# Kernel tuning notes

Hardware: AMD Instinct MI355X
Metric: run time of the kernel (lower is better)

## Reference

```python
import jax, jax.numpy as jnp
import numpy as np

N_NODES = 50000
N_EDGES = 800000
F_IN = 128
HID = 128
F_OUT = 2


def setup_inputs() -> dict:
    key = jax.random.key(0)
    ks = jax.random.split(key, 12)
    s = lambda d: 1.0 / np.sqrt(d)
    return {
        "x": jax.random.normal(ks[0], (N_NODES, F_IN), dtype=jnp.float32),
        "edge_index": jax.random.randint(ks[1], (2, N_EDGES), 0, N_NODES, dtype=jnp.int64),
        "W1_root": jax.random.normal(ks[2], (F_IN, HID), dtype=jnp.float32) * s(F_IN),
        "W1_nbr": jax.random.normal(ks[3], (F_IN, HID), dtype=jnp.float32) * s(F_IN),
        "b1": jnp.zeros((HID,), dtype=jnp.float32),
        "W2_root": jax.random.normal(ks[4], (HID, HID), dtype=jnp.float32) * s(HID),
        "W2_nbr": jax.random.normal(ks[5], (HID, HID), dtype=jnp.float32) * s(HID),
        "b2": jnp.zeros((HID,), dtype=jnp.float32),
        "Wa": jax.random.normal(ks[6], (HID, HID), dtype=jnp.float32) * s(HID),
        "a_src": jax.random.normal(ks[7], (HID,), dtype=jnp.float32) * s(HID),
        "a_dst": jax.random.normal(ks[8], (HID,), dtype=jnp.float32) * s(HID),
        "Wfc": jax.random.normal(ks[9], (HID, F_OUT), dtype=jnp.float32) * s(HID),
        "bfc": jnp.zeros((F_OUT,), dtype=jnp.float32),
    }


def reference(x, edge_index, W1_root, W1_nbr, b1, W2_root, W2_nbr, b2,
              Wa, a_src, a_dst, Wfc, bfc):
    src = edge_index[0]
    dst = edge_index[1]
    N = x.shape[0]

    def graph_conv(h, Wr, Wn, b):
        # sum-aggregate neighbor features, then two linear maps (PyG GraphConv)
        agg = jax.ops.segment_sum(h[src], dst, num_segments=N)  # [N, d]
        return h @ Wr + agg @ Wn + b

    h = jax.nn.relu(graph_conv(x, W1_root, W1_nbr, b1))
    h = jax.nn.relu(graph_conv(h, W2_root, W2_nbr, b2))

    # GAT-style attention: e_ij = LeakyReLU(a_src . Wh_j + a_dst . Wh_i)
    ht = h @ Wa                      # [N, HID]
    s_src = ht @ a_src               # [N]
    s_dst = ht @ a_dst               # [N]
    e = jax.nn.leaky_relu(s_src[src] + s_dst[dst], negative_slope=0.2)  # [E]

    # segment softmax over incoming edges of each destination node
    m = jax.ops.segment_max(e, dst, num_segments=N)          # [N]
    ee = jnp.exp(e - m[dst])                                  # [E]
    denom = jax.ops.segment_sum(ee, dst, num_segments=N)     # [N]
    alpha = ee / (denom[dst] + 1e-16)                         # [E]

    out = jax.ops.segment_sum(alpha[:, None] * ht[src], dst, num_segments=N)  # [N, HID]
    return out @ Wfc + bfc
```

## Files before the change

kernel.cpp:

```cpp
#include <hip/hip_runtime.h>
#include <cstddef>
#include <cstdint>


typedef __attribute__((ext_vector_type(8))) short short8;
typedef __attribute__((ext_vector_type(4))) float f32x4;

#define NBUK 128
#define BSH  9
#define CHUNK 1568

__device__ __forceinline__ ushort f2b(float f) {
  uint32_t u = __float_as_uint(f);
  u += 0x7fffu + ((u >> 16) & 1u);
  return (ushort)(u >> 16);
}
__device__ __forceinline__ float b2f(ushort h) {
  return __uint_as_float(((uint32_t)h) << 16);
}

__device__ __forceinline__ void gload_lds16(const void* g, void* l) {
  __builtin_amdgcn_global_load_lds(
      (const __attribute__((address_space(1))) void*)g,
      (__attribute__((address_space(3))) void*)l, 16, 0, 0);
}


__global__ __launch_bounds__(256) void split_kernel(
    const float* __restrict__ in, ushort* __restrict__ hi,
    ushort* __restrict__ lo, int n) {
  int i = (blockIdx.x * blockDim.x + threadIdx.x) * 8;
  if (i >= n) return;
  float4 v0 = *(const float4*)(in + i);
  float4 v1 = *(const float4*)(in + i + 4);
  float v[8] = {v0.x, v0.y, v0.z, v0.w, v1.x, v1.y, v1.z, v1.w};
  short8 h, l;
  #pragma unroll
  for (int b = 0; b < 8; ++b) {
    ushort hh = f2b(v[b]);
    h[b] = (short)hh;
    l[b] = (short)f2b(v[b] - b2f(hh));
  }
  *(short8*)(hi + i) = h;
  *(short8*)(lo + i) = l;
}


__global__ __launch_bounds__(256) void wsplit_kernel(
    const float* __restrict__ W0, const float* __restrict__ W1,
    const float* __restrict__ W2, const float* __restrict__ W3,
    const float* __restrict__ W4,
    ushort* __restrict__ WhT, ushort* __restrict__ WlT) {
  __shared__ float tile[128][128];
  int m = blockIdx.x;
  const float* W = (m == 0) ? W0 : (m == 1) ? W1 : (m == 2) ? W2 : (m == 3) ? W3 : W4;
  int t = threadIdx.x;
  #pragma unroll
  for (int i = 0; i < 64; ++i) {
    int idx = i * 256 + t;
    tile[idx >> 7][idx & 127] = W[idx];
  }
  __syncthreads();
  int j = t >> 1, k0 = (t & 1) * 64;
  size_t obase = (size_t)m * 16384 + (size_t)j * 128 + k0;
  #pragma unroll
  for (int c = 0; c < 8; ++c) {
    short8 h, l;
    #pragma unroll
    for (int b = 0; b < 8; ++b) {
      float v = tile[k0 + c * 8 + b][j];
      ushort hh = f2b(v);
      h[b] = (short)hh;
      l[b] = (short)f2b(v - b2f(hh));
    }
    *(short8*)(WhT + obase + c * 8) = h;
    *(short8*)(WlT + obase + c * 8) = l;
  }
}


__global__ __launch_bounds__(256) void bhist_kernel(
    const int* __restrict__ ei, int E, int* __restrict__ bcnt) {
  __shared__ int lh[NBUK];
  int t = threadIdx.x;
  if (t < NBUK) lh[t] = 0;
  __syncthreads();
  int base = blockIdx.x * CHUNK;
  int lim = base + CHUNK; if (lim > E) lim = E;
  for (int i = base + t; i < lim; i += 256) atomicAdd(&lh[ei[E + i] >> BSH], 1);
  __syncthreads();
  if (t < NBUK && lh[t]) atomicAdd(&bcnt[t], lh[t]);
}

__global__ __launch_bounds__(256) void bscan_kernel(
    const int* __restrict__ bcnt, int* __restrict__ bbase,
    int* __restrict__ gtail) {
  __shared__ int sA[NBUK], sB[NBUK];
  int t = threadIdx.x;
  if (t < NBUK) sA[t] = bcnt[t];
  __syncthreads();
  int *s = sA, *d = sB;
  for (int st = 1; st < NBUK; st <<= 1) {
    if (t < NBUK) d[t] = s[t] + ((t >= st) ? s[t - st] : 0);
    __syncthreads();
    int* tmp = s; s = d; d = tmp;
  }
  if (t < NBUK) {
    int exc = (t == 0) ? 0 : s[t - 1];
    bbase[t] = exc;
    gtail[t] = exc;
  }
  if (t == 0) bbase[NBUK] = s[NBUK - 1];
}

__global__ __launch_bounds__(256) void bscatter_kernel(
    const int* __restrict__ ei, int E, int* __restrict__ gtail,
    uint2* __restrict__ pair) {
  __shared__ int lh[NBUK], sB[NBUK], lofs[NBUK], lcur[NBUK], gbase[NBUK];
  __shared__ uint2 buf[CHUNK];
  int t = threadIdx.x;
  if (t < NBUK) lh[t] = 0;
  __syncthreads();
  int base = blockIdx.x * CHUNK;
  int lim = base + CHUNK; if (lim > E) lim = E;
  for (int i = base + t; i < lim; i += 256) atomicAdd(&lh[ei[E + i] >> BSH], 1);
  __syncthreads();
  int *s = lh, *d = sB;
  for (int st = 1; st < NBUK; st <<= 1) {
    if (t < NBUK) d[t] = s[t] + ((t >= st) ? s[t - st] : 0);
    __syncthreads();
    int* tmp = s; s = d; d = tmp;
  }
  if (t < NBUK) {
    lofs[t] = (t == 0) ? 0 : s[t - 1];
    lcur[t] = lofs[t];
  }
  __syncthreads();
  for (int i = base + t; i < lim; i += 256) {
    int srcv = ei[i], dstv = ei[E + i];
    int p = atomicAdd(&lcur[dstv >> BSH], 1);
    buf[p] = make_uint2((unsigned)srcv, (unsigned)dstv);
  }
  __syncthreads();
  if (t < NBUK) {
    int c = s[t] - lofs[t];
    gbase[t] = c ? atomicAdd(&gtail[t], c) : 0;
  }
  __syncthreads();
  int n = lim - base;
  for (int i = t; i < n; i += 256) {
    uint2 pr = buf[i];
    int b = ((int)pr.y) >> BSH;
    pair[gbase[b] + (i - lofs[b])] = pr;
  }
}

__global__ __launch_bounds__(256) void csrbuild_kernel(
    const uint2* __restrict__ pair, const int* __restrict__ bbase,
    int* __restrict__ ofs, int* __restrict__ csr, int N, int E) {
  __shared__ int hA[512], hB[512];
  int b = blockIdx.x, t = threadIdx.x;
  int base = bbase[b], cnt = bbase[b + 1] - base;
  int node0 = b << BSH;
  int nn = N - node0; if (nn > 512) nn = 512;
  hA[t] = 0; hA[t + 256] = 0;
  __syncthreads();
  for (int i = t; i < cnt; i += 256)
    atomicAdd(&hA[(int)pair[base + i].y - node0], 1);
  __syncthreads();
  int *s = hA, *d = hB;
  for (int st = 1; st < 512; st <<= 1) {
    #pragma unroll
    for (int k = 0; k < 2; ++k) {
      int i = t + k * 256;
      d[i] = s[i] + ((i >= st) ? s[i - st] : 0);
    }
    __syncthreads();
    int* tmp = s; s = d; d = tmp;
  }
  #pragma unroll
  for (int k = 0; k < 2; ++k) {
    int i = t + k * 256;
    if (i < nn) ofs[node0 + i] = base + (i == 0 ? 0 : s[i - 1]);
  }
  if (t == 0 && node0 + nn >= N) ofs[N] = E;
  #pragma unroll
  for (int k = 0; k < 2; ++k) {
    int i = t + k * 256;
    d[i] = (i == 0 ? 0 : s[i - 1]);
  }
  __syncthreads();
  for (int i = t; i < cnt; i += 256) {
    uint2 pr = pair[base + i];
    int p = atomicAdd(&d[(int)pr.y - node0], 1);
    csr[base + p] = (int)pr.x;
  }
}


__global__ __launch_bounds__(256) void agg_kernel(
    const ushort* __restrict__ Xh, const int* __restrict__ csr,
    const int* __restrict__ ofs, ushort* __restrict__ Gh,
    ushort* __restrict__ Gl, int N) {
  int node = (blockIdx.x * blockDim.x + threadIdx.x) >> 6;
  int lane = threadIdx.x & 63;
  if (node >= N) return;
  int g = lane >> 4, q = lane & 15;
  int beg = ofs[node], end = ofs[node + 1];
  float a[8] = {};
  for (int p = beg + g; p < end; p += 4) {
    int s = csr[p];
    short8 v = *(const short8*)(Xh + (size_t)s * 128 + q * 8);
    #pragma unroll
    for (int b = 0; b < 8; ++b) a[b] += b2f((ushort)v[b]);
  }
  #pragma unroll
  for (int b = 0; b < 8; ++b) {
    a[b] += __shfl_xor(a[b], 16);
    a[b] += __shfl_xor(a[b], 32);
  }
  if (lane < 16) {
    short8 h, l;
    #pragma unroll
    for (int b = 0; b < 8; ++b) {
      ushort hh = f2b(a[b]);
      h[b] = (short)hh;
      l[b] = (short)f2b(a[b] - b2f(hh));
    }
    *(short8*)(Gh + (size_t)node * 128 + q * 8) = h;
    *(short8*)(Gl + (size_t)node * 128 + q * 8) = l;
  }
}


template <int S, bool RELU, bool BIAS>
__global__ __launch_bounds__(512, 2) void mgemm_kernel(
    const ushort* __restrict__ A1h, const ushort* __restrict__ A1l,
    const ushort* __restrict__ A2h, const ushort* __restrict__ A2l,
    const ushort* __restrict__ WhT, const ushort* __restrict__ WlT,
    const float* __restrict__ bias,
    ushort* __restrict__ Ch, ushort* __restrict__ Cl, int M) {
  __shared__ char lds[2 * S * 16384];
  int t = threadIdx.x;
  int l = t & 63;
  int w = t >> 6;
  int j = (w << 4) + (l & 15);
  int krow0 = (l >> 4) * 8;
  int rowBase = blockIdx.x * 64;

  const ushort* srcs[4] = {A1h, A1l, (S > 1) ? A2h : A1h, (S > 1) ? A2l : A1l};
  int ldsWaveBase0 = (t & ~63) * 16;
  #pragma unroll
  for (int q = 0; q < 2 * S; ++q) {
    const char* gsrc = (const char*)srcs[q];
    #pragma unroll
    for (int part = 0; part < 2; ++part) {
      int c = part * 512 + t;
      int r = c >> 4;
      int cb = (c & 15) << 4;
      int row = rowBase + r;
      if (row >= M) row = M - 1;
      int sb = cb ^ ((r & 7) << 4);
      gload_lds16(gsrc + (size_t)row * 256 + sb,
                  &lds[q * 16384 + part * 8192 + ldsWaveBase0]);
    }
  }

  short8 wh[S][4], wl[S][4];
  #pragma unroll
  for (int s = 0; s < S; ++s) {
    #pragma unroll
    for (int ks = 0; ks < 4; ++ks) {
      size_t wb = (size_t)s * 16384 + (size_t)j * 128 + ks * 32 + krow0;
      wh[s][ks] = *(const short8*)(WhT + wb);
      wl[s][ks] = *(const short8*)(WlT + wb);
    }
  }

  __syncthreads();

  f32x4 acc[4];
  #pragma unroll
  for (int i = 0; i < 4; ++i) acc[i] = (f32x4){0.f, 0.f, 0.f, 0.f};

  #pragma unroll
  for (int rf = 0; rf < 4; ++rf) {
    int r = rf * 16 + (l & 15);
    int sw = (r & 7) << 4;
    int rb = r * 256;
    #pragma unroll
    for (int s = 0; s < S; ++s) {
      #pragma unroll
      for (int ks = 0; ks < 4; ++ks) {
        int off = rb + ((ks * 64 + (l >> 4) * 16) ^ sw);
        short8 ah = *(const short8*)&lds[(s * 2 + 0) * 16384 + off];
        short8 al = *(const short8*)&lds[(s * 2 + 1) * 16384 + off];
        acc[rf] = __builtin_amdgcn_mfma_f32_16x16x32_bf16(al, wh[s][ks], acc[rf], 0, 0, 0);
        acc[rf] = __builtin_amdgcn_mfma_f32_16x16x32_bf16(ah, wl[s][ks], acc[rf], 0, 0, 0);
        acc[rf] = __builtin_amdgcn_mfma_f32_16x16x32_bf16(ah, wh[s][ks], acc[rf], 0, 0, 0);
      }
    }
  }

  float bj = BIAS ? bias[j] : 0.f;
  #pragma unroll
  for (int rf = 0; rf < 4; ++rf) {
    int rbase = rowBase + rf * 16 + (l >> 4) * 4;
    #pragma unroll
    for (int r = 0; r < 4; ++r) {
      int row = rbase + r;
      if (row < M) {
        float v = acc[rf][r];
        if (BIAS) v += bj;
        if (RELU) v = fmaxf(v, 0.f);
        ushort h = f2b(v);
        Ch[(size_t)row * 128 + j] = h;
        Cl[(size_t)row * 128 + j] = f2b(v - b2f(h));
      }
    }
  }
}


__global__ __launch_bounds__(256) void dots_kernel(
    const ushort* __restrict__ HTh, const ushort* __restrict__ HTl,
    const float* __restrict__ a_src, const float* __restrict__ a_dst,
    float* __restrict__ ssrc, float* __restrict__ sdst, int N) {
  int n = (blockIdx.x * blockDim.x + threadIdx.x) >> 6;
  int lane = threadIdx.x & 63;
  if (n >= N) return;
  uint uh = ((const uint*)(HTh + (size_t)n * 128))[lane];
  uint ul = ((const uint*)(HTl + (size_t)n * 128))[lane];
  float h0 = b2f((ushort)(uh & 0xffff)) + b2f((ushort)(ul & 0xffff));
  float h1 = b2f((ushort)(uh >> 16)) + b2f((ushort)(ul >> 16));
  float vs = h0 * a_src[2 * lane] + h1 * a_src[2 * lane + 1];
  float vd = h0 * a_dst[2 * lane] + h1 * a_dst[2 * lane + 1];
  #pragma unroll
  for (int d = 32; d > 0; d >>= 1) {
    vs += __shfl_xor(vs, d);
    vd += __shfl_xor(vd, d);
  }
  if (lane == 0) { ssrc[n] = vs; sdst[n] = vd; }
}


__global__ __launch_bounds__(256) void attn_kernel(
    const ushort* __restrict__ HTh, const int* __restrict__ csr,
    const int* __restrict__ ofs, const float* __restrict__ ssrc,
    const float* __restrict__ sdst, float* __restrict__ outh, int N) {
  int n = (blockIdx.x * blockDim.x + threadIdx.x) >> 6;
  int lane = threadIdx.x & 63;
  if (n >= N) return;
  int beg = ofs[n], end = ofs[n + 1];
  float sd = sdst[n];

  float m = -3.4e38f, ssum = 0.f;
  for (int p = beg + lane; p < end; p += 64) {
    float e = ssrc[csr[p]] + sd;
    e = (e >= 0.f) ? e : 0.2f * e;
    float nm = fmaxf(m, e);
    ssum = ssum * __expf(m - nm) + __expf(e - nm);
    m = nm;
  }
  #pragma unroll
  for (int d = 32; d > 0; d >>= 1) {
    float om = __shfl_xor(m, d);
    float os = __shfl_xor(ssum, d);
    float nm = fmaxf(m, om);
    ssum = ssum * __expf(m - nm) + os * __expf(om - nm);
    m = nm;
  }
  float inv = 1.0f / (ssum + 1e-16f);

  int g = lane >> 4, q = lane & 15;
  float a[8] = {};
  for (int p = beg + g; p < end; p += 4) {
    int s = csr[p];
    float e = ssrc[s] + sd;
    e = (e >= 0.f) ? e : 0.2f * e;
    float wgt = __expf(e - m) * inv;
    short8 v = *(const short8*)(HTh + (size_t)s * 128 + q * 8);
    #pragma unroll
    for (int b = 0; b < 8; ++b) a[b] += wgt * b2f((ushort)v[b]);
  }
  #pragma unroll
  for (int b = 0; b < 8; ++b) {
    a[b] += __shfl_xor(a[b], 16);
    a[b] += __shfl_xor(a[b], 32);
  }
  if (lane < 16) {
    float4 o0 = {a[0], a[1], a[2], a[3]};
    float4 o1 = {a[4], a[5], a[6], a[7]};
    *(float4*)(outh + (size_t)n * 128 + q * 8) = o0;
    *(float4*)(outh + (size_t)n * 128 + q * 8 + 4) = o1;
  }
}


__global__ __launch_bounds__(256) void fc_kernel(
    const float* __restrict__ H, const float* __restrict__ Wfc,
    const float* __restrict__ bfc, float* __restrict__ out, int N) {
  int n = (blockIdx.x * blockDim.x + threadIdx.x) >> 6;
  int lane = threadIdx.x & 63;
  if (n >= N) return;
  float h0 = H[(size_t)n * 128 + lane];
  float h1 = H[(size_t)n * 128 + 64 + lane];
  float o0 = h0 * Wfc[lane * 2 + 0] + h1 * Wfc[(lane + 64) * 2 + 0];
  float o1 = h0 * Wfc[lane * 2 + 1] + h1 * Wfc[(lane + 64) * 2 + 1];
  #pragma unroll
  for (int d = 32; d > 0; d >>= 1) {
    o0 += __shfl_xor(o0, d);
    o1 += __shfl_xor(o1, d);
  }
  if (lane == 0) {
    out[(size_t)n * 2 + 0] = o0 + bfc[0];
    out[(size_t)n * 2 + 1] = o1 + bfc[1];
  }
}


static inline size_t align_up(size_t x, size_t a) { return (x + a - 1) & ~(a - 1); }

extern "C" void kernel_launch(void* const* d_in, const int* in_sizes, int n_in,
                              void* d_out, int out_size, void* d_ws, size_t ws_size,
                              hipStream_t stream) {
  const float* x     = (const float*)d_in[0];
  const int*   ei    = (const int*)d_in[1];
  const float* W1r   = (const float*)d_in[2];
  const float* W1n   = (const float*)d_in[3];
  const float* b1    = (const float*)d_in[4];
  const float* W2r   = (const float*)d_in[5];
  const float* W2n   = (const float*)d_in[6];
  const float* b2    = (const float*)d_in[7];
  const float* Wa    = (const float*)d_in[8];
  const float* a_src = (const float*)d_in[9];
  const float* a_dst = (const float*)d_in[10];
  const float* Wfc   = (const float*)d_in[11];
  const float* bfc   = (const float*)d_in[12];

  const int N = in_sizes[0] / 128;
  const int E = in_sizes[1] / 2;

  char* ws = (char*)d_ws;
  size_t off = 0;
  auto take = [&](size_t bytes) {
    char* p = ws + off;
    off = align_up(off + bytes, 256);
    return p;
  };
  const size_t NB = (size_t)N * 128 * 2;
  int*    ofs   = (int*)take((size_t)(N + 1) * 4);
  int*    csr   = (int*)take((size_t)E * 4);
  int*    bcnt  = (int*)take(NBUK * 4);
  int*    bbase = (int*)take((NBUK + 1) * 4);
  int*    gtail = (int*)take(NBUK * 4);
  uint2*  pair  = (uint2*)take((size_t)E * 8);
  float*  ssrc  = (float*)take((size_t)N * 4);
  float*  sdst  = (float*)take((size_t)N * 4);
  ushort* whT   = (ushort*)take((size_t)5 * 16384 * 2);
  ushort* wlT   = (ushort*)take((size_t)5 * 16384 * 2);
  ushort* bA    = (ushort*)take(NB);
  ushort* bB    = (ushort*)take(NB);
  ushort* bC    = (ushort*)take(NB);
  ushort* bD    = (ushort*)take(NB);
  ushort* bE    = (ushort*)take(NB);
  ushort* bF    = (ushort*)take(NB);
  float*  outh  = (float*)bE;

  hipMemsetAsync(bcnt, 0, NBUK * 4, stream);

  const int nodeBlocks = (N + 3) / 4;
  const int gemmBlocks = (N + 63) / 64;
  const int splitBlocks = (N * 128 / 8 + 255) / 256;
  const int chunkBlocks = (E + CHUNK - 1) / CHUNK;
  const int bukBlocks   = (N + 511) / 512;

  wsplit_kernel<<<5, 256, 0, stream>>>(W1r, W1n, W2r, W2n, Wa, whT, wlT);
  split_kernel<<<splitBlocks, 256, 0, stream>>>(x, bA, bB, N * 128);
  bhist_kernel<<<chunkBlocks, 256, 0, stream>>>(ei, E, bcnt);
  bscan_kernel<<<1, 256, 0, stream>>>(bcnt, bbase, gtail);
  bscatter_kernel<<<chunkBlocks, 256, 0, stream>>>(ei, E, gtail, pair);
  csrbuild_kernel<<<bukBlocks, 256, 0, stream>>>(pair, bbase, ofs, csr, N, E);

  agg_kernel<<<nodeBlocks, 256, 0, stream>>>(bA, csr, ofs, bC, bD, N);
  mgemm_kernel<2, true, true><<<gemmBlocks, 512, 0, stream>>>(
      bA, bB, bC, bD, whT, wlT, b1, bE, bF, N);

  agg_kernel<<<nodeBlocks, 256, 0, stream>>>(bE, csr, ofs, bC, bD, N);
  mgemm_kernel<2, true, true><<<gemmBlocks, 512, 0, stream>>>(
      bE, bF, bC, bD, whT + 2 * 16384, wlT + 2 * 16384, b2, bA, bB, N);

  mgemm_kernel<1, false, false><<<gemmBlocks, 512, 0, stream>>>(
      bA, bB, nullptr, nullptr, whT + 4 * 16384, wlT + 4 * 16384,
      nullptr, bC, bD, N);
  dots_kernel<<<nodeBlocks, 256, 0, stream>>>(bC, bD, a_src, a_dst, ssrc, sdst, N);
  attn_kernel<<<nodeBlocks, 256, 0, stream>>>(bC, csr, ofs, ssrc, sdst, outh, N);

  fc_kernel<<<nodeBlocks, 256, 0, stream>>>(outh, Wfc, bfc, (float*)d_out, N);
}
```

Measured before the change: 281.6 us.

## Fuse final FC into attention kernel, cache edge scores in LDS, prefetch gathers

Fuses the output linear layer into the attention kernel: each wave reduces its 128-wide aggregate against Wfc with 16-lane shuffles and writes the two outputs directly. This removes the fp32 [N,128] intermediate write and its re-read plus one launch. The softmax becomes two passes: a max pass, then an exp/sum pass, with per-edge scores and exponentials cached in shared memory for the first 128 edges so the weighted gather skips recomputation. Both gather loops in agg and attn software-pipeline the next neighbor row load, at the cost of extra registers.

```diff
diff --git a/kernel.cpp b/kernel.cpp
--- a/kernel.cpp
+++ b/kernel.cpp
@@ -208,9 +208,17 @@
   int g = lane >> 4, q = lane & 15;
   int beg = ofs[node], end = ofs[node + 1];
   float a[8] = {};
-  for (int p = beg + g; p < end; p += 4) {
+  int p = beg + g;
+  if (p < end) {
     int s = csr[p];
     short8 v = *(const short8*)(Xh + (size_t)s * 128 + q * 8);
+    for (p += 4; p < end; p += 4) {
+      int s2 = csr[p];
+      short8 v2 = *(const short8*)(Xh + (size_t)s2 * 128 + q * 8);
+      #pragma unroll
+      for (int b = 0; b < 8; ++b) a[b] += b2f((ushort)v[b]);
+      v = v2;
+    }
     #pragma unroll
     for (int b = 0; b < 8; ++b) a[b] += b2f((ushort)v[b]);
   }
@@ -347,39 +355,72 @@
 __global__ __launch_bounds__(256) void attn_kernel(
     const ushort* __restrict__ HTh, const int* __restrict__ csr,
     const int* __restrict__ ofs, const float* __restrict__ ssrc,
-    const float* __restrict__ sdst, float* __restrict__ outh, int N) {
+    const float* __restrict__ sdst, const float* __restrict__ Wfc,
+    const float* __restrict__ bfc, float* __restrict__ out, int N) {
+  __shared__ float eld[4][128];
+  int wv = (threadIdx.x >> 6) & 3;
   int n = (blockIdx.x * blockDim.x + threadIdx.x) >> 6;
   int lane = threadIdx.x & 63;
   if (n >= N) return;
   int beg = ofs[n], end = ofs[n + 1];
+  int deg = end - beg;
   float sd = sdst[n];
 
-  float m = -3.4e38f, ssum = 0.f;
-  for (int p = beg + lane; p < end; p += 64) {
-    float e = ssrc[csr[p]] + sd;
+  float m = -3.4e38f;
+  for (int i = lane; i < deg; i += 64) {
+    float e = ssrc[csr[beg + i]] + sd;
     e = (e >= 0.f) ? e : 0.2f * e;
-    float nm = fmaxf(m, e);
-    ssum = ssum * __expf(m - nm) + __expf(e - nm);
-    m = nm;
-  }
-  #pragma unroll
-  for (int d = 32; d > 0; d >>= 1) {
-    float om = __shfl_xor(m, d);
-    float os = __shfl_xor(ssum, d);
-    float nm = fmaxf(m, om);
-    ssum = ssum * __expf(m - nm) + os * __expf(om - nm);
-    m = nm;
-  }
+    if (i < 128) eld[wv][i] = e;
+    m = fmaxf(m, e);
+  }
+  #pragma unroll
+  for (int d = 32; d > 0; d >>= 1) m = fmaxf(m, __shfl_xor(m, d));
+
+  float ssum = 0.f;
+  for (int i = lane; i < deg; i += 64) {
+    float e;
+    if (i < 128) e = eld[wv][i];
+    else {
+      e = ssrc[csr[beg + i]] + sd;
+      e = (e >= 0.f) ? e : 0.2f * e;
+    }
+    float t = __expf(e - m);
+    if (i < 128) eld[wv][i] = t;
+    ssum += t;
+  }
+  #pragma unroll
+  for (int d = 32; d > 0; d >>= 1) ssum += __shfl_xor(ssum, d);
   float inv = 1.0f / (ssum + 1e-16f);
 
   int g = lane >> 4, q = lane & 15;
   float a[8] = {};
-  for (int p = beg + g; p < end; p += 4) {
-    int s = csr[p];
-    float e = ssrc[s] + sd;
-    e = (e >= 0.f) ? e : 0.2f * e;
-    float wgt = __expf(e - m) * inv;
+  int i = g;
+  if (i < deg) {
+    int s = csr[beg + i];
     short8 v = *(const short8*)(HTh + (size_t)s * 128 + q * 8);
+    float t;
+    if (i < 128) t = eld[wv][i];
+    else {
+      float e = ssrc[s] + sd;
+      e = (e >= 0.f) ? e : 0.2f * e;
+      t = __expf(e - m);
+    }
+    for (i += 4; i < deg; i += 4) {
+      int s2 = csr[beg + i];
+      short8 v2 = *(const short8*)(HTh + (size_t)s2 * 128 + q * 8);
+      float t2;
+      if (i < 128) t2 = eld[wv][i];
+      else {
+        float e2 = ssrc[s2] + sd;
+        e2 = (e2 >= 0.f) ? e2 : 0.2f * e2;
+        t2 = __expf(e2 - m);
+      }
+      float wgt = t * inv;
+      #pragma unroll
+      for (int b = 0; b < 8; ++b) a[b] += wgt * b2f((ushort)v[b]);
+      v = v2; t = t2;
+    }
+    float wgt = t * inv;
     #pragma unroll
     for (int b = 0; b < 8; ++b) a[b] += wgt * b2f((ushort)v[b]);
   }
@@ -388,27 +429,17 @@
     a[b] += __shfl_xor(a[b], 16);
     a[b] += __shfl_xor(a[b], 32);
   }
-  if (lane < 16) {
-    float4 o0 = {a[0], a[1], a[2], a[3]};
-    float4 o1 = {a[4], a[5], a[6], a[7]};
-    *(float4*)(outh + (size_t)n * 128 + q * 8) = o0;
-    *(float4*)(outh + (size_t)n * 128 + q * 8 + 4) = o1;
-  }
-}
-
-
-__global__ __launch_bounds__(256) void fc_kernel(
-    const float* __restrict__ H, const float* __restrict__ Wfc,
-    const float* __restrict__ bfc, float* __restrict__ out, int N) {
-  int n = (blockIdx.x * blockDim.x + threadIdx.x) >> 6;
-  int lane = threadIdx.x & 63;
-  if (n >= N) return;
-  float h0 = H[(size_t)n * 128 + lane];
-  float h1 = H[(size_t)n * 128 + 64 + lane];
-  float o0 = h0 * Wfc[lane * 2 + 0] + h1 * Wfc[(lane + 64) * 2 + 0];
-  float o1 = h0 * Wfc[lane * 2 + 1] + h1 * Wfc[(lane + 64) * 2 + 1];
-  #pragma unroll
-  for (int d = 32; d > 0; d >>= 1) {
+
+  float4 wf0 = *(const float4*)(Wfc + q * 16);
+  float4 wf1 = *(const float4*)(Wfc + q * 16 + 4);
+  float4 wf2 = *(const float4*)(Wfc + q * 16 + 8);
+  float4 wf3 = *(const float4*)(Wfc + q * 16 + 12);
+  float o0 = a[0] * wf0.x + a[1] * wf0.z + a[2] * wf1.x + a[3] * wf1.z +
+             a[4] * wf2.x + a[5] * wf2.z + a[6] * wf3.x + a[7] * wf3.z;
+  float o1 = a[0] * wf0.y + a[1] * wf0.w + a[2] * wf1.y + a[3] * wf1.w +
+             a[4] * wf2.y + a[5] * wf2.w + a[6] * wf3.y + a[7] * wf3.w;
+  #pragma unroll
+  for (int d = 1; d < 16; d <<= 1) {
     o0 += __shfl_xor(o0, d);
     o1 += __shfl_xor(o1, d);
   }
@@ -465,7 +496,6 @@
   ushort* bD    = (ushort*)take(NB);
   ushort* bE    = (ushort*)take(NB);
   ushort* bF    = (ushort*)take(NB);
-  float*  outh  = (float*)bE;
 
   hipMemsetAsync(bcnt, 0, NBUK * 4, stream);
 
@@ -494,7 +524,7 @@
       bA, bB, nullptr, nullptr, whT + 4 * 16384, wlT + 4 * 16384,
       nullptr, bC, bD, N);
   dots_kernel<<<nodeBlocks, 256, 0, stream>>>(bC, bD, a_src, a_dst, ssrc, sdst, N);
-  attn_kernel<<<nodeBlocks, 256, 0, stream>>>(bC, csr, ofs, ssrc, sdst, outh, N);
-
-  fc_kernel<<<nodeBlocks, 256, 0, stream>>>(outh, Wfc, bfc, (float*)d_out, N);
-}
+
+  attn_kernel<<<nodeBlocks, 256, 0, stream>>>(
+      bC, csr, ofs, ssrc, sdst, Wfc, bfc, (float*)d_out, N);
+}
```

New measurement: 263.4 us. 1.07x faster.
